# Optimization experiments

Measured on AMD Instinct MI355X. Metric: run time of the kernel, lower is better.

Reference implementation:

```python
import jax, jax.numpy as jnp
import numpy as np

N_NODES = 50000
N_EDGES = 800000
IN_DIM = 128
HEADS = 4
OUT_DIM = 16
HD = HEADS * OUT_DIM  # 64
EDGE_DIM = 1
NEG_SLOPE = 0.2


def setup_inputs() -> dict:
    key = jax.random.key(0)
    ks = jax.random.split(key, 12)
    x = jax.random.normal(ks[0], (N_NODES, IN_DIM), dtype=jnp.float32)
    edge_index = jax.random.randint(ks[1], (2, N_EDGES), 0, N_NODES, dtype=jnp.int64)
    edge_attr = jax.random.uniform(ks[2], (N_EDGES, EDGE_DIM), dtype=jnp.float32)
    s = 0.1
    Wl = jax.random.normal(ks[3], (IN_DIM, HD), dtype=jnp.float32) * s
    bl = jax.random.normal(ks[4], (HD,), dtype=jnp.float32) * s
    Wr = jax.random.normal(ks[5], (IN_DIM, HD), dtype=jnp.float32) * s
    br = jax.random.normal(ks[6], (HD,), dtype=jnp.float32) * s
    We = jax.random.normal(ks[7], (EDGE_DIM, HD), dtype=jnp.float32) * s
    att = jax.random.normal(ks[8], (HEADS, OUT_DIM), dtype=jnp.float32) * s
    bias_out = jax.random.normal(ks[9], (HD,), dtype=jnp.float32) * s
    Wres = jax.random.normal(ks[10], (IN_DIM, HD), dtype=jnp.float32) * s
    bres = jax.random.normal(ks[11], (HD,), dtype=jnp.float32) * s
    return {"x": x, "edge_index": edge_index, "edge_attr": edge_attr,
            "Wl": Wl, "bl": bl, "Wr": Wr, "br": br, "We": We,
            "att": att, "bias_out": bias_out, "Wres": Wres, "bres": bres}


def _gatv2_layer(x, edge_index, edge_attr, Wl, bl, Wr, br, We, att, bias_out, Wres, bres):
    src, dst = edge_index[0], edge_index[1]
    # projections: [N, H, D]
    x_l = (x @ Wl + bl).reshape(N_NODES, HEADS, OUT_DIM)
    x_r = (x @ Wr + br).reshape(N_NODES, HEADS, OUT_DIM)
    edge_emb = (edge_attr @ We).reshape(N_EDGES, HEADS, OUT_DIM)
    # per-edge attention score (GATv2): a^T LeakyReLU(x_l[src] + x_r[dst] + e)
    x_j = x_l[src]                                   # [E, H, D] gather (source message)
    feat = x_j + x_r[dst] + edge_emb                 # [E, H, D]
    score = jnp.einsum('ehd,hd->eh', jax.nn.leaky_relu(feat, NEG_SLOPE), att)  # [E, H]
    # segment softmax over destination neighborhoods
    m = jax.ops.segment_max(score, dst, num_segments=N_NODES)   # [N, H]
    ex = jnp.exp(score - m[dst])                                 # [E, H]
    denom = jax.ops.segment_sum(ex, dst, num_segments=N_NODES)  # [N, H]
    alpha = ex / (denom[dst] + 1e-16)                            # [E, H]
    # scatter-add aggregation of weighted source messages
    out = jax.ops.segment_sum(alpha[:, :, None] * x_j, dst, num_segments=N_NODES)  # [N, H, D]
    out = out.reshape(N_NODES, HD) + bias_out        # concat heads + conv bias
    # residual (in_dim != out_features -> linear projection), then ELU
    out = out + (x @ Wres + bres)
    out = jax.nn.elu(out)
    return out, edge_index, alpha


def reference(x, edge_index, edge_attr, Wl, bl, Wr, br, We, att, bias_out, Wres, bres):
    return _gatv2_layer(x, edge_index, edge_attr, Wl, bl, Wr, br, We, att, bias_out, Wres, bres)
```

## Files before the change

kernel.cpp:

```cpp
#include <hip/hip_runtime.h>
#include <math.h>

#define N_NODES 50000
#define N_EDGES 800000
#define IN_DIM  128
#define HEADS   4
#define OUT_DIM 16
#define HD      64
#define NEG_SLOPE 0.2f
#define CAP     128

__global__ void k0_zero(int* __restrict__ count) {
    int i = blockIdx.x * blockDim.x + threadIdx.x;
    if (i < N_NODES) count[i] = 0;
}

__global__ __launch_bounds__(256)
void k1_proj(const float* __restrict__ x,
             const float* __restrict__ Wl, const float* __restrict__ bl,
             const float* __restrict__ Wr, const float* __restrict__ br,
             const float* __restrict__ Wres, const float* __restrict__ bres,
             float* __restrict__ xl, float* __restrict__ xr,
             float* __restrict__ xres) {
    __shared__ float xs[16][IN_DIM];
    const int base = blockIdx.x * 16;
    {
        const float4* s4 = (const float4*)(x + (size_t)base * IN_DIM);
        float4* d4 = (float4*)&xs[0][0];
        for (int i = threadIdx.x; i < 16 * IN_DIM / 4; i += 256) d4[i] = s4[i];
    }
    __syncthreads();

    const int group = threadIdx.x >> 6;
    const int col   = threadIdx.x & 63;

    float al0 = 0, al1 = 0, al2 = 0, al3 = 0;
    float ar0 = 0, ar1 = 0, ar2 = 0, ar3 = 0;
    float as0 = 0, as1 = 0, as2 = 0, as3 = 0;
#pragma unroll 4
    for (int k = 0; k < IN_DIM; ++k) {
        const float wl = Wl[k * HD + col];
        const float wr = Wr[k * HD + col];
        const float ws = Wres[k * HD + col];
        const float x0 = xs[group * 4 + 0][k];
        const float x1 = xs[group * 4 + 1][k];
        const float x2 = xs[group * 4 + 2][k];
        const float x3 = xs[group * 4 + 3][k];
        al0 += x0 * wl; al1 += x1 * wl; al2 += x2 * wl; al3 += x3 * wl;
        ar0 += x0 * wr; ar1 += x1 * wr; ar2 += x2 * wr; ar3 += x3 * wr;
        as0 += x0 * ws; as1 += x1 * ws; as2 += x2 * ws; as3 += x3 * ws;
    }
    const float blv = bl[col], brv = br[col], bsv = bres[col];
    const size_t n0 = (size_t)(base + group * 4) * HD + col;
    xl[n0 + 0 * HD] = al0 + blv; xl[n0 + 1 * HD] = al1 + blv;
    xl[n0 + 2 * HD] = al2 + blv; xl[n0 + 3 * HD] = al3 + blv;
    xr[n0 + 0 * HD] = ar0 + brv; xr[n0 + 1 * HD] = ar1 + brv;
    xr[n0 + 2 * HD] = ar2 + brv; xr[n0 + 3 * HD] = ar3 + brv;
    xres[n0 + 0 * HD] = as0 + bsv; xres[n0 + 1 * HD] = as1 + bsv;
    xres[n0 + 2 * HD] = as2 + bsv; xres[n0 + 3 * HD] = as3 + bsv;
}

__global__ __launch_bounds__(256)
void k2_hist(const int* __restrict__ dst, int* __restrict__ count) {
    int e = blockIdx.x * blockDim.x + threadIdx.x;
    if (e < N_EDGES) atomicAdd(&count[dst[e]], 1);
}

#define SCAN_BLOCKS 196

__global__ __launch_bounds__(256)
void k3a_scan1(const int* __restrict__ count, int* __restrict__ incl,
               int* __restrict__ bsum) {
    __shared__ int s[256];
    const int t = threadIdx.x;
    const int i = blockIdx.x * 256 + t;
    int c = (i < N_NODES) ? count[i] : 0;
    s[t] = c;
    __syncthreads();
    for (int off = 1; off < 256; off <<= 1) {
        int v = (t >= off) ? s[t - off] : 0;
        __syncthreads();
        s[t] += v;
        __syncthreads();
    }
    if (i < N_NODES) incl[i] = s[t];
    if (t == 255) bsum[blockIdx.x] = s[255];
}

__global__ __launch_bounds__(256)
void k3b_scan2(int* __restrict__ bsum, int* __restrict__ boff) {
    __shared__ int s[256];
    const int t = threadIdx.x;
    int c = (t < SCAN_BLOCKS) ? bsum[t] : 0;
    s[t] = c;
    __syncthreads();
    for (int off = 1; off < 256; off <<= 1) {
        int v = (t >= off) ? s[t - off] : 0;
        __syncthreads();
        s[t] += v;
        __syncthreads();
    }
    if (t < SCAN_BLOCKS) boff[t] = s[t] - c;
}

__global__ __launch_bounds__(256)
void k3c_scan3(const int* __restrict__ count, int* __restrict__ incl ,
               const int* __restrict__ boff, int* __restrict__ cursor) {
    const int i = blockIdx.x * 256 + threadIdx.x;
    if (i >= N_NODES) return;
    const int v = incl[i] - count[i] + boff[blockIdx.x];
    incl[i] = v;
    cursor[i] = v;
}

__global__ __launch_bounds__(256)
void k4_scatter(const int* __restrict__ src, const int* __restrict__ dst,
                const float* __restrict__ ea,
                int* __restrict__ cursor, int* __restrict__ eid,
                int* __restrict__ src_s, float* __restrict__ ea_s,
                float* __restrict__ out_ei) {
    int e = blockIdx.x * blockDim.x + threadIdx.x;
    if (e >= N_EDGES) return;
    const int d = dst[e];
    const int s = src[e];
    const int pos = atomicAdd(&cursor[d], 1);
    eid[pos] = e;
    src_s[pos] = s;
    ea_s[pos] = ea[e];
    out_ei[e] = (float)s;
    out_ei[N_EDGES + e] = (float)d;
}

__global__ __launch_bounds__(256)
void k5_node(const int* __restrict__ src_s, const float* __restrict__ ea_s,
             const int* __restrict__ rowptr, const int* __restrict__ count,
             const int* __restrict__ eid,
             const float* __restrict__ xl, const float* __restrict__ xr,
             const float* __restrict__ xres,
             const float* __restrict__ We, const float* __restrict__ att,
             const float* __restrict__ bias_out,
             float* __restrict__ out, float* __restrict__ out_alpha) {
    __shared__ float sc_lds[4][CAP][HEADS];

    const int wv   = threadIdx.x >> 6;
    const int lane = threadIdx.x & 63;
    const int u    = lane & 15;
    const int g    = lane >> 4;
    const int n    = blockIdx.x * 4 + wv;

    const int base = rowptr[n];
    const int deg  = count[n];

    const float4 xr4 = *(const float4*)(xr  + (size_t)n * HD + 4 * u);
    const float4 We4 = *(const float4*)(We  + 4 * u);
    const float4 at4 = *(const float4*)(att + 4 * u);

    float m = -INFINITY, dsum = 0.f;
    float4 acc = make_float4(0.f, 0.f, 0.f, 0.f);

    for (int c0 = 0; c0 < deg; c0 += 64) {
        const int nrem = min(64, deg - c0);
        int s_my = 0; float a_my = 0.f;
        if (lane < nrem) {
            s_my = src_s[base + c0 + lane];
            a_my = ea_s[base + c0 + lane];
        }
        const int nchunk = (nrem + 3) >> 2;

        int   j   = g;
        bool  v   = j < nrem;
        int   s   = __shfl(s_my, j);
        float aev = __shfl(a_my, j);
        float4 xlv = make_float4(0.f, 0.f, 0.f, 0.f);
        if (v) xlv = *(const float4*)(xl + (size_t)s * HD + 4 * u);

        for (int c = 0; c < nchunk; ++c) {
            const float4 cur  = xlv;
            const bool   curv = v;
            const float  ca   = aev;
            const int    cj   = 4 * c + g;
            j = 4 * (c + 1) + g;
            v = j < nrem;
            s   = __shfl(s_my, j & 63);
            aev = __shfl(a_my, j & 63);
            if (v) xlv = *(const float4*)(xl + (size_t)s * HD + 4 * u);

            if (curv) {
                float f0 = cur.x + xr4.x + ca * We4.x;
                float f1 = cur.y + xr4.y + ca * We4.y;
                float f2 = cur.z + xr4.z + ca * We4.z;
                float f3 = cur.w + xr4.w + ca * We4.w;
                f0 = f0 > 0.f ? f0 : NEG_SLOPE * f0;
                f1 = f1 > 0.f ? f1 : NEG_SLOPE * f1;
                f2 = f2 > 0.f ? f2 : NEG_SLOPE * f2;
                f3 = f3 > 0.f ? f3 : NEG_SLOPE * f3;
                float p = f0 * at4.x + f1 * at4.y + f2 * at4.z + f3 * at4.w;
                p += __shfl_xor(p, 1);
                p += __shfl_xor(p, 2);
                const int jj = c0 + cj;
                if (jj < CAP && (u & 3) == 0) sc_lds[wv][jj][u >> 2] = p;
                const float mnew = fmaxf(m, p);
                const float scl  = __expf(m - mnew);
                const float pe   = __expf(p - mnew);
                dsum  = dsum * scl + pe;
                acc.x = acc.x * scl + pe * cur.x;
                acc.y = acc.y * scl + pe * cur.y;
                acc.z = acc.z * scl + pe * cur.z;
                acc.w = acc.w * scl + pe * cur.w;
                m = mnew;
            }
        }
    }

#pragma unroll
    for (int off = 16; off <= 32; off <<= 1) {
        const float mo = __shfl_xor(m, off);
        const float d2 = __shfl_xor(dsum, off);
        float4 a2;
        a2.x = __shfl_xor(acc.x, off);
        a2.y = __shfl_xor(acc.y, off);
        a2.z = __shfl_xor(acc.z, off);
        a2.w = __shfl_xor(acc.w, off);
        const float mm = fmaxf(m, mo);
        const float s1 = (m  == -INFINITY) ? 0.f : __expf(m - mm);
        const float s2 = (mo == -INFINITY) ? 0.f : __expf(mo - mm);
        dsum  = dsum * s1 + d2 * s2;
        acc.x = acc.x * s1 + a2.x * s2;
        acc.y = acc.y * s1 + a2.y * s2;
        acc.z = acc.z * s1 + a2.z * s2;
        acc.w = acc.w * s1 + a2.w * s2;
        m = mm;
    }
    const float inv = 1.f / (dsum + 1e-16f);

    const float m0 = __shfl(m, 0),  m1 = __shfl(m, 4);
    const float m2 = __shfl(m, 8),  m3 = __shfl(m, 12);
    const float i0 = __shfl(inv, 0), i1 = __shfl(inv, 4);
    const float i2 = __shfl(inv, 8), i3 = __shfl(inv, 12);

    __syncthreads();

    for (int jj = lane; jj < deg; jj += 64) {
        const int e = eid[base + jj];
        float s0, s1, s2, s3;
        if (jj < CAP) {
            s0 = sc_lds[wv][jj][0]; s1 = sc_lds[wv][jj][1];
            s2 = sc_lds[wv][jj][2]; s3 = sc_lds[wv][jj][3];
        } else {
            const int   sN  = src_s[base + jj];
            const float aev = ea_s[base + jj];
            float sc[4];
            for (int h2 = 0; h2 < 4; ++h2) {
                float a2 = 0.f;
                for (int d2 = 0; d2 < 16; ++d2) {
                    const int hd2 = h2 * 16 + d2;
                    float f = xl[(size_t)sN * HD + hd2] + xr[(size_t)n * HD + hd2]
                              + aev * We[hd2];
                    f = f > 0.f ? f : NEG_SLOPE * f;
                    a2 += f * att[hd2];
                }
                sc[h2] = a2;
            }
            s0 = sc[0]; s1 = sc[1]; s2 = sc[2]; s3 = sc[3];
        }
        float4 a4;
        a4.x = __expf(s0 - m0) * i0;
        a4.y = __expf(s1 - m1) * i1;
        a4.z = __expf(s2 - m2) * i2;
        a4.w = __expf(s3 - m3) * i3;
        *(float4*)(out_alpha + (size_t)e * HEADS) = a4;
    }

    if (g == 0) {
        const float4 xs4 = *(const float4*)(xres + (size_t)n * HD + 4 * u);
        const float4 b4  = *(const float4*)(bias_out + 4 * u);
        float4 o;
        o.x = acc.x * inv + b4.x + xs4.x;
        o.y = acc.y * inv + b4.y + xs4.y;
        o.z = acc.z * inv + b4.z + xs4.z;
        o.w = acc.w * inv + b4.w + xs4.w;
        o.x = o.x > 0.f ? o.x : __expf(o.x) - 1.f;
        o.y = o.y > 0.f ? o.y : __expf(o.y) - 1.f;
        o.z = o.z > 0.f ? o.z : __expf(o.z) - 1.f;
        o.w = o.w > 0.f ? o.w : __expf(o.w) - 1.f;
        *(float4*)(out + (size_t)n * HD + 4 * u) = o;
    }
}

extern "C" void kernel_launch(void* const* d_in, const int* in_sizes, int n_in,
                              void* d_out, int out_size, void* d_ws, size_t ws_size,
                              hipStream_t stream) {
    const float* x        = (const float*)d_in[0];
    const int*   ei       = (const int*)d_in[1];
    const float* ea       = (const float*)d_in[2];
    const float* Wl       = (const float*)d_in[3];
    const float* bl       = (const float*)d_in[4];
    const float* Wr       = (const float*)d_in[5];
    const float* br       = (const float*)d_in[6];
    const float* We       = (const float*)d_in[7];
    const float* att      = (const float*)d_in[8];
    const float* bias_out = (const float*)d_in[9];
    const float* Wres     = (const float*)d_in[10];
    const float* bres     = (const float*)d_in[11];

    const int* src = ei;
    const int* dst = ei + N_EDGES;

    float* out       = (float*)d_out;
    float* out_ei    = out + (size_t)N_NODES * HD;
    float* out_alpha = out_ei + 2 * (size_t)N_EDGES;

    float* ws   = (float*)d_ws;
    float* xl   = ws;
    float* xr   = xl + (size_t)N_NODES * HD;
    float* xres = xr + (size_t)N_NODES * HD;
    float* ea_s = xres + (size_t)N_NODES * HD;
    int* ibuf   = (int*)(ea_s + N_EDGES);
    int* count  = ibuf;
    int* rowptr = count + N_NODES;
    int* cursor = rowptr + N_NODES;
    int* bsum   = cursor + N_NODES;
    int* boff   = bsum + SCAN_BLOCKS;
    int* eid    = boff + SCAN_BLOCKS;
    int* src_s  = eid + N_EDGES;

    k0_zero<<<SCAN_BLOCKS, 256, 0, stream>>>(count);
    k1_proj<<<N_NODES / 16, 256, 0, stream>>>(x, Wl, bl, Wr, br, Wres, bres,
                                              xl, xr, xres);
    k2_hist<<<N_EDGES / 256, 256, 0, stream>>>(dst, count);
    k3a_scan1<<<SCAN_BLOCKS, 256, 0, stream>>>(count, rowptr, bsum);
    k3b_scan2<<<1, 256, 0, stream>>>(bsum, boff);
    k3c_scan3<<<SCAN_BLOCKS, 256, 0, stream>>>(count, rowptr, boff, cursor);
    k4_scatter<<<N_EDGES / 256, 256, 0, stream>>>(src, dst, ea, cursor, eid,
                                                  src_s, ea_s, out_ei);
    k5_node<<<N_NODES / 4, 256, 0, stream>>>(src_s, ea_s, rowptr, count, eid,
                                             xl, xr, xres, We, att, bias_out,
                                             out, out_alpha);
}
```

Before: 299.9 us.

## Fuse histogram into projection, pack edge records, use exp2 online softmax

The dst histogram atomics move into the projection kernel, one edge per thread (3125 blocks × 256 threads = 800000), so the separate histogram launch goes away. The three sorted per-edge arrays (eid, src, edge_attr) become one int4 record, so each edge is read with a single 16-byte load. The online softmax works in base 2 with the hardware exp2 instruction and a single-exp update, and the projection loop reads x from shared memory as float4. Together these cut kernel launches, scattered memory transactions and transcendental work, at the cost of a wider 16-byte record write per edge in the scatter.

```diff
diff --git a/kernel.cpp b/kernel.cpp
--- a/kernel.cpp
+++ b/kernel.cpp
@@ -9,6 +9,11 @@
 #define HD      64
 #define NEG_SLOPE 0.2f
 #define CAP     128
+#define LOG2E   1.44269504088896340736f
+
+__device__ __forceinline__ float hw_exp2(float x) {
+    return __builtin_amdgcn_exp2f(x);
+}
 
 __global__ void k0_zero(int* __restrict__ count) {
     int i = blockIdx.x * blockDim.x + threadIdx.x;
@@ -20,10 +25,14 @@
              const float* __restrict__ Wl, const float* __restrict__ bl,
              const float* __restrict__ Wr, const float* __restrict__ br,
              const float* __restrict__ Wres, const float* __restrict__ bres,
+             const int* __restrict__ dst, int* __restrict__ count,
              float* __restrict__ xl, float* __restrict__ xr,
              float* __restrict__ xres) {
     __shared__ float xs[16][IN_DIM];
     const int base = blockIdx.x * 16;
+
+    atomicAdd(&count[dst[blockIdx.x * 256 + threadIdx.x]], 1);
+
     {
         const float4* s4 = (const float4*)(x + (size_t)base * IN_DIM);
         float4* d4 = (float4*)&xs[0][0];
@@ -34,36 +43,34 @@
     const int group = threadIdx.x >> 6;
     const int col   = threadIdx.x & 63;
 
-    float al0 = 0, al1 = 0, al2 = 0, al3 = 0;
-    float ar0 = 0, ar1 = 0, ar2 = 0, ar3 = 0;
-    float as0 = 0, as1 = 0, as2 = 0, as3 = 0;
-#pragma unroll 4
-    for (int k = 0; k < IN_DIM; ++k) {
-        const float wl = Wl[k * HD + col];
-        const float wr = Wr[k * HD + col];
-        const float ws = Wres[k * HD + col];
-        const float x0 = xs[group * 4 + 0][k];
-        const float x1 = xs[group * 4 + 1][k];
-        const float x2 = xs[group * 4 + 2][k];
-        const float x3 = xs[group * 4 + 3][k];
-        al0 += x0 * wl; al1 += x1 * wl; al2 += x2 * wl; al3 += x3 * wl;
-        ar0 += x0 * wr; ar1 += x1 * wr; ar2 += x2 * wr; ar3 += x3 * wr;
-        as0 += x0 * ws; as1 += x1 * ws; as2 += x2 * ws; as3 += x3 * ws;
+    float al[4] = {0, 0, 0, 0}, ar[4] = {0, 0, 0, 0}, as[4] = {0, 0, 0, 0};
+    for (int k0 = 0; k0 < IN_DIM; k0 += 4) {
+        float xv[4][4];
+        *(float4*)xv[0] = *(const float4*)&xs[group * 4 + 0][k0];
+        *(float4*)xv[1] = *(const float4*)&xs[group * 4 + 1][k0];
+        *(float4*)xv[2] = *(const float4*)&xs[group * 4 + 2][k0];
+        *(float4*)xv[3] = *(const float4*)&xs[group * 4 + 3][k0];
+#pragma unroll
+        for (int kk = 0; kk < 4; ++kk) {
+            const float wl = Wl[(k0 + kk) * HD + col];
+            const float wr = Wr[(k0 + kk) * HD + col];
+            const float ws = Wres[(k0 + kk) * HD + col];
+#pragma unroll
+            for (int i = 0; i < 4; ++i) {
+                al[i] += xv[i][kk] * wl;
+                ar[i] += xv[i][kk] * wr;
+                as[i] += xv[i][kk] * ws;
+            }
+        }
     }
     const float blv = bl[col], brv = br[col], bsv = bres[col];
     const size_t n0 = (size_t)(base + group * 4) * HD + col;
-    xl[n0 + 0 * HD] = al0 + blv; xl[n0 + 1 * HD] = al1 + blv;
-    xl[n0 + 2 * HD] = al2 + blv; xl[n0 + 3 * HD] = al3 + blv;
-    xr[n0 + 0 * HD] = ar0 + brv; xr[n0 + 1 * HD] = ar1 + brv;
-    xr[n0 + 2 * HD] = ar2 + brv; xr[n0 + 3 * HD] = ar3 + brv;
-    xres[n0 + 0 * HD] = as0 + bsv; xres[n0 + 1 * HD] = as1 + bsv;
-    xres[n0 + 2 * HD] = as2 + bsv; xres[n0 + 3 * HD] = as3 + bsv;
-}
-
-__global__ __launch_bounds__(256)
-void k2_hist(const int* __restrict__ dst, int* __restrict__ count) {
-    int e = blockIdx.x * blockDim.x + threadIdx.x;
-    if (e < N_EDGES) atomicAdd(&count[dst[e]], 1);
+#pragma unroll
+    for (int i = 0; i < 4; ++i) {
+        xl[n0 + i * HD]   = al[i] + blv;
+        xr[n0 + i * HD]   = ar[i] + brv;
+        xres[n0 + i * HD] = as[i] + bsv;
+    }
 }
 
 #define SCAN_BLOCKS 196
@@ -116,25 +123,21 @@
 __global__ __launch_bounds__(256)
 void k4_scatter(const int* __restrict__ src, const int* __restrict__ dst,
                 const float* __restrict__ ea,
-                int* __restrict__ cursor, int* __restrict__ eid,
-                int* __restrict__ src_s, float* __restrict__ ea_s,
+                int* __restrict__ cursor, int4* __restrict__ recs,
                 float* __restrict__ out_ei) {
     int e = blockIdx.x * blockDim.x + threadIdx.x;
     if (e >= N_EDGES) return;
     const int d = dst[e];
     const int s = src[e];
     const int pos = atomicAdd(&cursor[d], 1);
-    eid[pos] = e;
-    src_s[pos] = s;
-    ea_s[pos] = ea[e];
+    recs[pos] = make_int4(e, s, __float_as_int(ea[e]), 0);
     out_ei[e] = (float)s;
     out_ei[N_EDGES + e] = (float)d;
 }
 
 __global__ __launch_bounds__(256)
-void k5_node(const int* __restrict__ src_s, const float* __restrict__ ea_s,
+void k5_node(const int4* __restrict__ recs,
              const int* __restrict__ rowptr, const int* __restrict__ count,
-             const int* __restrict__ eid,
              const float* __restrict__ xl, const float* __restrict__ xr,
              const float* __restrict__ xres,
              const float* __restrict__ We, const float* __restrict__ att,
@@ -153,7 +156,8 @@
 
     const float4 xr4 = *(const float4*)(xr  + (size_t)n * HD + 4 * u);
     const float4 We4 = *(const float4*)(We  + 4 * u);
-    const float4 at4 = *(const float4*)(att + 4 * u);
+    float4 at4       = *(const float4*)(att + 4 * u);
+    at4.x *= LOG2E; at4.y *= LOG2E; at4.z *= LOG2E; at4.w *= LOG2E;
 
     float m = -INFINITY, dsum = 0.f;
     float4 acc = make_float4(0.f, 0.f, 0.f, 0.f);
@@ -162,8 +166,9 @@
         const int nrem = min(64, deg - c0);
         int s_my = 0; float a_my = 0.f;
         if (lane < nrem) {
-            s_my = src_s[base + c0 + lane];
-            a_my = ea_s[base + c0 + lane];
+            const int4 r = recs[base + c0 + lane];
+            s_my = r.y;
+            a_my = __int_as_float(r.z);
         }
         const int nchunk = (nrem + 3) >> 2;
 
@@ -199,15 +204,16 @@
                 p += __shfl_xor(p, 2);
                 const int jj = c0 + cj;
                 if (jj < CAP && (u & 3) == 0) sc_lds[wv][jj][u >> 2] = p;
-                const float mnew = fmaxf(m, p);
-                const float scl  = __expf(m - mnew);
-                const float pe   = __expf(p - mnew);
+                const float t    = hw_exp2(-fabsf(p - m));
+                const bool  up   = (p >= m);
+                const float scl  = up ? t : 1.f;
+                const float pe   = up ? 1.f : t;
+                m = fmaxf(m, p);
                 dsum  = dsum * scl + pe;
                 acc.x = acc.x * scl + pe * cur.x;
                 acc.y = acc.y * scl + pe * cur.y;
                 acc.z = acc.z * scl + pe * cur.z;
                 acc.w = acc.w * scl + pe * cur.w;
-                m = mnew;
             }
         }
     }
@@ -222,8 +228,8 @@
         a2.z = __shfl_xor(acc.z, off);
         a2.w = __shfl_xor(acc.w, off);
         const float mm = fmaxf(m, mo);
-        const float s1 = (m  == -INFINITY) ? 0.f : __expf(m - mm);
-        const float s2 = (mo == -INFINITY) ? 0.f : __expf(mo - mm);
+        const float s1 = (m  == -INFINITY) ? 0.f : hw_exp2(m - mm);
+        const float s2 = (mo == -INFINITY) ? 0.f : hw_exp2(mo - mm);
         dsum  = dsum * s1 + d2 * s2;
         acc.x = acc.x * s1 + a2.x * s2;
         acc.y = acc.y * s1 + a2.y * s2;
@@ -241,14 +247,15 @@
     __syncthreads();
 
     for (int jj = lane; jj < deg; jj += 64) {
-        const int e = eid[base + jj];
+        const int4 r = recs[base + jj];
+        const int  e = r.x;
         float s0, s1, s2, s3;
         if (jj < CAP) {
-            s0 = sc_lds[wv][jj][0]; s1 = sc_lds[wv][jj][1];
-            s2 = sc_lds[wv][jj][2]; s3 = sc_lds[wv][jj][3];
+            const float4 sc4 = *(const float4*)&sc_lds[wv][jj][0];
+            s0 = sc4.x; s1 = sc4.y; s2 = sc4.z; s3 = sc4.w;
         } else {
-            const int   sN  = src_s[base + jj];
-            const float aev = ea_s[base + jj];
+            const int   sN  = r.y;
+            const float aev = __int_as_float(r.z);
             float sc[4];
             for (int h2 = 0; h2 < 4; ++h2) {
                 float a2 = 0.f;
@@ -259,15 +266,15 @@
                     f = f > 0.f ? f : NEG_SLOPE * f;
                     a2 += f * att[hd2];
                 }
-                sc[h2] = a2;
+                sc[h2] = a2 * LOG2E;
             }
             s0 = sc[0]; s1 = sc[1]; s2 = sc[2]; s3 = sc[3];
         }
         float4 a4;
-        a4.x = __expf(s0 - m0) * i0;
-        a4.y = __expf(s1 - m1) * i1;
-        a4.z = __expf(s2 - m2) * i2;
-        a4.w = __expf(s3 - m3) * i3;
+        a4.x = hw_exp2(s0 - m0) * i0;
+        a4.y = hw_exp2(s1 - m1) * i1;
+        a4.z = hw_exp2(s2 - m2) * i2;
+        a4.w = hw_exp2(s3 - m3) * i3;
         *(float4*)(out_alpha + (size_t)e * HEADS) = a4;
     }
 
@@ -314,26 +321,25 @@
     float* xl   = ws;
     float* xr   = xl + (size_t)N_NODES * HD;
     float* xres = xr + (size_t)N_NODES * HD;
-    float* ea_s = xres + (size_t)N_NODES * HD;
-    int* ibuf   = (int*)(ea_s + N_EDGES);
+    int* ibuf   = (int*)(xres + (size_t)N_NODES * HD);
     int* count  = ibuf;
     int* rowptr = count + N_NODES;
     int* cursor = rowptr + N_NODES;
     int* bsum   = cursor + N_NODES;
     int* boff   = bsum + SCAN_BLOCKS;
-    int* eid    = boff + SCAN_BLOCKS;
-    int* src_s  = eid + N_EDGES;
+    size_t recoff = (size_t)(boff + SCAN_BLOCKS - (int*)d_ws);
+    recoff = (recoff + 3) & ~(size_t)3;
+    int4* recs  = (int4*)((int*)d_ws + recoff);
 
     k0_zero<<<SCAN_BLOCKS, 256, 0, stream>>>(count);
     k1_proj<<<N_NODES / 16, 256, 0, stream>>>(x, Wl, bl, Wr, br, Wres, bres,
-                                              xl, xr, xres);
-    k2_hist<<<N_EDGES / 256, 256, 0, stream>>>(dst, count);
+                                              dst, count, xl, xr, xres);
     k3a_scan1<<<SCAN_BLOCKS, 256, 0, stream>>>(count, rowptr, bsum);
     k3b_scan2<<<1, 256, 0, stream>>>(bsum, boff);
     k3c_scan3<<<SCAN_BLOCKS, 256, 0, stream>>>(count, rowptr, boff, cursor);
-    k4_scatter<<<N_EDGES / 256, 256, 0, stream>>>(src, dst, ea, cursor, eid,
-                                                  src_s, ea_s, out_ei);
-    k5_node<<<N_NODES / 4, 256, 0, stream>>>(src_s, ea_s, rowptr, count, eid,
+    k4_scatter<<<(N_EDGES + 255) / 256, 256, 0, stream>>>(src, dst, ea, cursor,
+                                                          recs, out_ei);
+    k5_node<<<N_NODES / 4, 256, 0, stream>>>(recs, rowptr, count,
                                              xl, xr, xres, We, att, bias_out,
                                              out, out_alpha);
 }
```

After: 310.8 us. 3.7% more time.
